# Kernel tuning notes

Measured on AMD Instinct MI355X. Metric: run time of the kernel, lower is better.

The kernel has to match this reference:

```python
import jax, jax.numpy as jnp
import numpy as np

B, T, M, PH, PW = 4, 8, 128, 48, 48
QD, CD, H, DH = 1024, 768, 8, 64
INNER = H * DH

def layer_norm(x, g, b, eps=1e-5):
    m = x.mean(-1, keepdims=True)
    v = ((x - m) ** 2).mean(-1, keepdims=True)
    return (x - m) * jax.lax.rsqrt(v + eps) * g + b

def setup_inputs():
    key = jax.random.key(0)
    ks = jax.random.split(key, 10)
    x = jax.random.normal(ks[0], (B * T, PH * PW, QD), jnp.float32)
    context = jax.random.normal(ks[1], (B, M, CD), jnp.float32)
    sg_node_positions = jax.random.normal(ks[2], (B, M, 3), jnp.float32) * 2.0
    # valid c2w: identity rotation + random translation (invertible)
    c2w = jnp.broadcast_to(jnp.eye(4, dtype=jnp.float32), (B, T, 4, 4))
    camera_c2w = c2w.at[..., :3, 3].set(jax.random.normal(ks[3], (B, T, 3), jnp.float32))
    intrinsics = jnp.broadcast_to(jnp.array([[1.0, 0.0, 0.5], [0.0, 1.0, 0.5], [0.0, 0.0, 1.0]], jnp.float32), (B, 3, 3))
    s = 0.02
    Wq = jax.random.normal(ks[4], (QD, INNER), jnp.float32) * s
    Wk = jax.random.normal(ks[5], (CD, INNER), jnp.float32) * s
    Wv = jax.random.normal(ks[6], (CD, INNER), jnp.float32) * s
    Wo = jax.random.normal(ks[7], (INNER, QD), jnp.float32) * s
    gate = jnp.array([0.1], jnp.float32)          # zero-init in module; nonzero so path is active
    spatial_gate = jnp.array([0.1], jnp.float32)
    spatial_log_sigma = jax.random.normal(ks[8], (H,), jnp.float32) * 0.1
    depth_log_alpha = jax.random.normal(ks[9], (H,), jnp.float32) * 0.1
    gamma_q = jnp.ones((QD,), jnp.float32); beta_q = jnp.zeros((QD,), jnp.float32)
    gamma_k = jnp.ones((CD,), jnp.float32); beta_k = jnp.zeros((CD,), jnp.float32)
    return dict(x=x, context=context, sg_node_positions=sg_node_positions, camera_c2w=camera_c2w,
                intrinsics=intrinsics, Wq=Wq, Wk=Wk, Wv=Wv, Wo=Wo, gate=gate, spatial_gate=spatial_gate,
                spatial_log_sigma=spatial_log_sigma, depth_log_alpha=depth_log_alpha,
                gamma_q=gamma_q, beta_q=beta_q, gamma_k=gamma_k, beta_k=beta_k,
                patch_h=PH, patch_w=PW)

def spatial_bias(sg_node_positions, camera_c2w, intrinsics, spatial_log_sigma, depth_log_alpha, patch_h, patch_w):
    Bb, Mn, _ = sg_node_positions.shape
    Tn = camera_c2w.shape[1]
    w2c = jnp.linalg.inv(camera_c2w)
    R = w2c[:, :, :3, :3]
    tv = w2c[:, :, :3, 3]
    p_cam = jnp.einsum('btij,bmj->btmi', R, sg_node_positions) + tv[:, :, None, :]  # (B,T,M,3)
    z = jnp.clip(p_cam[..., 2], 1e-4, None)
    fx = intrinsics[:, 0, 0]; fy = intrinsics[:, 1, 1]
    cx = intrinsics[:, 0, 2]; cy = intrinsics[:, 1, 2]
    u = fx[:, None, None] * (p_cam[..., 0] / z) + cx[:, None, None]   # (B,T,M)
    v = fy[:, None, None] * (p_cam[..., 1] / z) + cy[:, None, None]
    gy = (jnp.arange(patch_h, dtype=jnp.float32) + 0.5) / patch_h
    gx = (jnp.arange(patch_w, dtype=jnp.float32) + 0.5) / patch_w
    gyy, gxx = jnp.meshgrid(gy, gx, indexing='ij')
    gxx = gxx.reshape(-1); gyy = gyy.reshape(-1)                       # (P,)
    sq = (gxx[None, None, :, None] - u[:, :, None, :]) ** 2 + (gyy[None, None, :, None] - v[:, :, None, :]) ** 2  # (B,T,P,M)
    sigma = jnp.exp(spatial_log_sigma)
    inv2s = z[:, :, None, :] ** 2 / (2.0 * sigma[None, None, :, None] ** 2 + 1e-8)  # (B,T,H,M)
    bias = -sq[:, :, None, :, :] * inv2s[:, :, :, None, :]             # (B,T,H,P,M)
    depth_term = depth_log_alpha[None, None, :, None, None] * (-jnp.log(z))[:, :, None, None, :]
    bias = bias + depth_term
    behind = p_cam[..., 2] <= 0.0
    bias = jnp.where(behind[:, :, None, None, :], 0.0, bias)
    return bias.reshape(Bb * Tn, bias.shape[2], patch_h * patch_w, Mn)  # (BT,H,P,M)

def reference(x, context, sg_node_positions, camera_c2w, intrinsics, Wq, Wk, Wv, Wo, gate, spatial_gate,
              spatial_log_sigma, depth_log_alpha, gamma_q, beta_q, gamma_k, beta_k, patch_h, patch_w):
    BT, P, _ = x.shape
    Bb, Mn, _ = context.shape
    Tn = camera_c2w.shape[1]
    q = layer_norm(x, gamma_q, beta_q) @ Wq                            # (BT,P,INNER)
    ck = layer_norm(context, gamma_k, beta_k)
    k = ck @ Wk
    v = ck @ Wv
    q = q.reshape(BT, P, H, DH).transpose(0, 2, 1, 3)                  # (BT,H,P,DH)
    k = jnp.broadcast_to(k.reshape(Bb, 1, Mn, H, DH), (Bb, Tn, Mn, H, DH)).reshape(BT, Mn, H, DH).transpose(0, 2, 1, 3)
    v = jnp.broadcast_to(v.reshape(Bb, 1, Mn, H, DH), (Bb, Tn, Mn, H, DH)).reshape(BT, Mn, H, DH).transpose(0, 2, 1, 3)
    scores = jnp.einsum('bhpd,bhmd->bhpm', q, k) * (DH ** -0.5)        # (BT,H,P,M)
    bias = spatial_bias(sg_node_positions, camera_c2w, intrinsics, spatial_log_sigma, depth_log_alpha, patch_h, patch_w)
    scores = scores + jnp.tanh(spatial_gate) * bias
    attn = jax.nn.softmax(scores, axis=-1)
    out = jnp.einsum('bhpm,bhmd->bhpd', attn, v).transpose(0, 2, 1, 3).reshape(BT, P, INNER)
    return x + jnp.tanh(gate) * (out @ Wo)
```

## Files before the change

### kernel.cpp

```cpp
#include <hip/hip_runtime.h>
#include <hip/hip_bf16.h>
#include <stdint.h>
#include <cstddef>

typedef short short8 __attribute__((ext_vector_type(8)));
typedef float f32x4 __attribute__((ext_vector_type(4)));
typedef unsigned short us4 __attribute__((ext_vector_type(4)));
typedef unsigned short us8 __attribute__((ext_vector_type(8)));

#define DEV static __device__ __forceinline__

DEV unsigned short f2b(float f) {
  __hip_bfloat16 h = __float2bfloat16(f);
  return __builtin_bit_cast(unsigned short, h);
}

DEV void gload_lds16(const void* g, void* lds) {
  __builtin_amdgcn_global_load_lds((const __attribute__((address_space(1))) unsigned int*)g,
                                   (__attribute__((address_space(3))) unsigned int*)lds, 16, 0, 0);
}

template<int EPI>
__launch_bounds__(256, 2)
__global__ void gemm_bt(const unsigned short* __restrict__ A,
                        const unsigned short* __restrict__ Bt,
                        unsigned short* __restrict__ Cb,
                        float* __restrict__ Cf,
                        const float* __restrict__ xres,
                        const float* __restrict__ gatep,
                        int M, int N, int K)
{
  __shared__ __attribute__((aligned(16))) char As[16384];
  __shared__ __attribute__((aligned(16))) char Bs[16384];
  const int tid  = threadIdx.x;
  const int lane = tid & 63, w = tid >> 6;
  const int wr = w >> 1, wc = w & 1;
  const int g = lane >> 4, lr = lane & 15;
  const int ntile = N >> 7;
  const int nwg = gridDim.x;
  const int bid = blockIdx.x;
  const int tile = ((nwg & 7) == 0) ? ((bid & 7)*(nwg >> 3) + (bid >> 3)) : bid;
  const int m0 = (tile / ntile) << 7;
  const int n0 = (tile % ntile) << 7;

  const int lrow  = lane >> 3;
  const int lslot = (lane & 7) ^ lrow;

  f32x4 acc[4][4] = {};

  for (int k0 = 0; k0 < K; k0 += 64) {
#pragma unroll
    for (int c = 0; c < 4; ++c) {
      const int rowc = (w*4 + c)*8;
      gload_lds16(A  + (size_t)(m0 + rowc + lrow)*K + k0 + lslot*8, As + rowc*128);
      gload_lds16(Bt + (size_t)(n0 + rowc + lrow)*K + k0 + lslot*8, Bs + rowc*128);
    }
    __syncthreads();
#pragma unroll
    for (int ks = 0; ks < 2; ++ks) {
      short8 af[4], bfr[4];
#pragma unroll
      for (int mt = 0; mt < 4; ++mt) {
        int row = wr*64 + mt*16 + lr;
        int slot = (ks*4 + g) ^ (row & 7);
        af[mt] = *(const short8*)(As + row*128 + slot*16);
      }
#pragma unroll
      for (int nt = 0; nt < 4; ++nt) {
        int row = wc*64 + nt*16 + lr;
        int slot = (ks*4 + g) ^ (row & 7);
        bfr[nt] = *(const short8*)(Bs + row*128 + slot*16);
      }
#pragma unroll
      for (int mt = 0; mt < 4; ++mt)
#pragma unroll
        for (int nt = 0; nt < 4; ++nt)
          acc[mt][nt] = __builtin_amdgcn_mfma_f32_16x16x32_bf16(af[mt], bfr[nt], acc[mt][nt], 0, 0, 0);
    }
    __syncthreads();
  }

  float* Sw = (float*)(As) + w*1024;
  if (EPI == 1) {
    const float tg = tanhf(gatep[0]);
#pragma unroll
    for (int mt = 0; mt < 4; ++mt) {
#pragma unroll
      for (int nt = 0; nt < 4; ++nt)
#pragma unroll
        for (int r = 0; r < 4; ++r)
          Sw[(g*4 + r)*64 + nt*16 + lr] = acc[mt][nt][r];
#pragma unroll
      for (int rep = 0; rep < 4; ++rep) {
        int row2 = rep*4 + g;
        int colf = lr*4;
        f32x4 val = *(const f32x4*)(Sw + row2*64 + colf);
        size_t rowg = (size_t)(m0 + wr*64 + mt*16 + row2);
        size_t idx = rowg * (size_t)N + (n0 + wc*64 + colf);
        f32x4 xv = *(const f32x4*)(xres + idx);
#pragma unroll
        for (int j = 0; j < 4; ++j) val[j] = xv[j] + tg*val[j];
        *(f32x4*)(Cf + idx) = val;
      }
    }
  } else {
#pragma unroll
    for (int mt = 0; mt < 4; ++mt) {
#pragma unroll
      for (int nt = 0; nt < 4; ++nt)
#pragma unroll
        for (int r = 0; r < 4; ++r)
          Sw[(g*4 + r)*64 + nt*16 + lr] = acc[mt][nt][r];
#pragma unroll
      for (int rep = 0; rep < 2; ++rep) {
        int row2 = rep*8 + (lane >> 3);
        int colf = (lane & 7)*8;
        f32x4 a0 = *(const f32x4*)(Sw + row2*64 + colf);
        f32x4 a1 = *(const f32x4*)(Sw + row2*64 + colf + 4);
        us8 ov;
#pragma unroll
        for (int j = 0; j < 4; ++j) { ov[j] = f2b(a0[j]); ov[4+j] = f2b(a1[j]); }
        size_t rowg = (size_t)(m0 + wr*64 + mt*16 + row2);
        *(us8*)(Cb + rowg * (size_t)N + (n0 + wc*64 + colf)) = ov;
      }
    }
  }
}

__launch_bounds__(256, 2)
__global__ void gemm_kv(const unsigned short* __restrict__ ck,
                        const unsigned short* __restrict__ Wk_t,
                        const unsigned short* __restrict__ Wv_t,
                        unsigned short* __restrict__ Kb,
                        unsigned short* __restrict__ Vt)
{
  __shared__ __attribute__((aligned(16))) char As[16384];
  __shared__ __attribute__((aligned(16))) char Bs[16384];
  const int bid = blockIdx.x;
  const int kv = bid >> 4, bidl = bid & 15;
  const unsigned short* Bt = kv ? Wv_t : Wk_t;
  const int m0 = (bidl >> 2) << 7, n0 = (bidl & 3) << 7;
  const int tid  = threadIdx.x;
  const int lane = tid & 63, w = tid >> 6;
  const int wr = w >> 1, wc = w & 1;
  const int g = lane >> 4, lr = lane & 15;
  const int lrow  = lane >> 3;
  const int lslot = (lane & 7) ^ lrow;
  const int K = 768;

  f32x4 acc[4][4] = {};

  for (int k0 = 0; k0 < K; k0 += 64) {
#pragma unroll
    for (int c = 0; c < 4; ++c) {
      const int rowc = (w*4 + c)*8;
      gload_lds16(ck + (size_t)(m0 + rowc + lrow)*K + k0 + lslot*8, As + rowc*128);
      gload_lds16(Bt + (size_t)(n0 + rowc + lrow)*K + k0 + lslot*8, Bs + rowc*128);
    }
    __syncthreads();
#pragma unroll
    for (int ks = 0; ks < 2; ++ks) {
      short8 af[4], bfr[4];
#pragma unroll
      for (int mt = 0; mt < 4; ++mt) {
        int row = wr*64 + mt*16 + lr;
        int slot = (ks*4 + g) ^ (row & 7);
        af[mt] = *(const short8*)(As + row*128 + slot*16);
      }
#pragma unroll
      for (int nt = 0; nt < 4; ++nt) {
        int row = wc*64 + nt*16 + lr;
        int slot = (ks*4 + g) ^ (row & 7);
        bfr[nt] = *(const short8*)(Bs + row*128 + slot*16);
      }
#pragma unroll
      for (int mt = 0; mt < 4; ++mt)
#pragma unroll
        for (int nt = 0; nt < 4; ++nt)
          acc[mt][nt] = __builtin_amdgcn_mfma_f32_16x16x32_bf16(af[mt], bfr[nt], acc[mt][nt], 0, 0, 0);
    }
    __syncthreads();
  }

#pragma unroll
  for (int mt = 0; mt < 4; ++mt)
#pragma unroll
    for (int nt = 0; nt < 4; ++nt)
#pragma unroll
      for (int r = 0; r < 4; ++r) {
        int row = m0 + wr*64 + mt*16 + g*4 + r;
        int col = n0 + wc*64 + nt*16 + lr;
        int bb = row >> 7, mm = row & 127, hh = col >> 6, dd = col & 63;
        unsigned short val = f2b(acc[mt][nt][r]);
        if (kv == 0) Kb[(((size_t)(bb*8 + hh))*128 + mm)*64 + dd] = val;
        else         Vt[(((size_t)(bb*8 + hh))*64 + dd)*128 + mm] = val;
      }
}

template<int NSEG>
__global__ void ln_rows(const float* __restrict__ in, const float* __restrict__ gamma,
                        const float* __restrict__ beta, unsigned short* __restrict__ out, int C)
{
  const int lane = threadIdx.x & 63;
  const size_t row = (size_t)blockIdx.x*4 + (threadIdx.x >> 6);
  const float* rp = in + row * (size_t)C;
  f32x4 vals[NSEG];
  float s = 0.f, sq = 0.f;
#pragma unroll
  for (int i = 0; i < NSEG; ++i) {
    f32x4 v = *(const f32x4*)(rp + (i*64 + lane)*4);
    vals[i] = v;
#pragma unroll
    for (int j = 0; j < 4; ++j) { s += v[j]; sq += v[j]*v[j]; }
  }
#pragma unroll
  for (int off = 32; off >= 1; off >>= 1) {
    s  += __shfl_xor(s, off);
    sq += __shfl_xor(sq, off);
  }
  const float invC = 1.0f / (float)C;
  float mean = s * invC;
  float var  = sq * invC - mean*mean;
  float rstd = rsqrtf(var + 1e-5f);
#pragma unroll
  for (int i = 0; i < NSEG; ++i) {
    int cb = (i*64 + lane)*4;
    f32x4 gm = *(const f32x4*)(gamma + cb);
    f32x4 bb = *(const f32x4*)(beta + cb);
    us4 ov;
#pragma unroll
    for (int j = 0; j < 4; ++j)
      ov[j] = f2b((vals[i][j] - mean)*rstd*gm[j] + bb[j]);
    *(us4*)(out + row * (size_t)C + cb) = ov;
  }
}

__global__ void transpose_all(const float* __restrict__ Wq, const float* __restrict__ Wk,
                              const float* __restrict__ Wv, const float* __restrict__ Wo,
                              unsigned short* __restrict__ Wq_t, unsigned short* __restrict__ Wk_t,
                              unsigned short* __restrict__ Wv_t, unsigned short* __restrict__ Wo_t)
{
  __shared__ float tile[32][33];
  int bidx = blockIdx.x;
  const float* src; unsigned short* dst; int R, C;
  if (bidx < 512)       { src = Wq; dst = Wq_t; R = 1024; C = 512; }
  else if (bidx < 896)  { src = Wk; dst = Wk_t; R = 768;  C = 512;  bidx -= 512; }
  else if (bidx < 1280) { src = Wv; dst = Wv_t; R = 768;  C = 512;  bidx -= 896; }
  else                  { src = Wo; dst = Wo_t; R = 512;  C = 1024; bidx -= 1280; }
  const int cb = C >> 5;
  const int bx = bidx % cb, by = bidx / cb;
  const int tx = threadIdx.x & 31, ty = threadIdx.x >> 5;
#pragma unroll
  for (int i = 0; i < 32; i += 8)
    tile[ty + i][tx] = src[(size_t)(by*32 + ty + i)*C + bx*32 + tx];
  __syncthreads();
#pragma unroll
  for (int i = 0; i < 32; i += 8)
    dst[(size_t)(bx*32 + ty + i)*R + by*32 + tx] = f2b(tile[tx][ty + i]);
}

__global__ void spatial_pre(const float* __restrict__ pos, const float* __restrict__ c2w,
                            const float* __restrict__ intr, const float* __restrict__ sls,
                            const float* __restrict__ dla,
                            float* __restrict__ u_o, float* __restrict__ v_o, float* __restrict__ bh_o,
                            float* __restrict__ iv_o, float* __restrict__ dp_o)
{
  const int bt = blockIdx.x;
  const int b = bt >> 3;
  const int m = threadIdx.x;
  const float* Mc = c2w + (size_t)bt*16;
  float r00=Mc[0], r01=Mc[1], r02=Mc[2],  t0=Mc[3];
  float r10=Mc[4], r11=Mc[5], r12=Mc[6],  t1=Mc[7];
  float r20=Mc[8], r21=Mc[9], r22=Mc[10], t2=Mc[11];
  float a00 = r11*r22 - r12*r21;
  float a01 = r02*r21 - r01*r22;
  float a02 = r01*r12 - r02*r11;
  float a10 = r12*r20 - r10*r22;
  float a11 = r00*r22 - r02*r20;
  float a12 = r02*r10 - r00*r12;
  float a20 = r10*r21 - r11*r20;
  float a21 = r01*r20 - r00*r21;
  float a22 = r00*r11 - r01*r10;
  float det = r00*a00 + r01*a10 + r02*a20;
  float id = 1.0f/det;
  a00*=id; a01*=id; a02*=id; a10*=id; a11*=id; a12*=id; a20*=id; a21*=id; a22*=id;
  float tv0 = -(a00*t0 + a01*t1 + a02*t2);
  float tv1 = -(a10*t0 + a11*t1 + a12*t2);
  float tv2 = -(a20*t0 + a21*t1 + a22*t2);
  const float* pm = pos + (size_t)(b*128 + m)*3;
  float px = pm[0], py = pm[1], pz = pm[2];
  float x = a00*px + a01*py + a02*pz + tv0;
  float y = a10*px + a11*py + a12*pz + tv1;
  float zraw = a20*px + a21*py + a22*pz + tv2;
  float z = fmaxf(zraw, 1e-4f);
  float fx = intr[b*9 + 0], fy = intr[b*9 + 4], cx = intr[b*9 + 2], cy = intr[b*9 + 5];
  u_o[bt*128 + m] = fx*(x/z) + cx;
  v_o[bt*128 + m] = fy*(y/z) + cy;
  bh_o[bt*128 + m] = (zraw <= 0.0f) ? 1.0f : 0.0f;
  float lz = __logf(z);
#pragma unroll
  for (int hh = 0; hh < 8; ++hh) {
    float sg = __expf(sls[hh]);
    iv_o[(size_t)(bt*8 + hh)*128 + m] = z*z / (2.0f*sg*sg + 1e-8f);
    dp_o[(size_t)(bt*8 + hh)*128 + m] = dla[hh] * (-lz);
  }
}

__launch_bounds__(256, 2)
__global__ void attn_kernel(const unsigned short* __restrict__ q,
                            const unsigned short* __restrict__ Kb,
                            const unsigned short* __restrict__ Vt,
                            const float* __restrict__ ub, const float* __restrict__ vb,
                            const float* __restrict__ bhb,
                            const float* __restrict__ ivb, const float* __restrict__ dpb,
                            const float* __restrict__ sgate,
                            unsigned short* __restrict__ out)
{
  const int bid = blockIdx.x;
  const int ptile = bid % 18;
  const int h  = (bid / 18) & 7;
  const int bt = bid / (18*8);
  const int b  = bt >> 3;
  const int lane = threadIdx.x & 63, w = threadIdx.x >> 6;
  const int g = lane >> 4, lr = lane & 15;
  const int p0 = ptile*128 + w*32;

  const float sg = tanhf(sgate[0]);
  const unsigned short* Kh = Kb + ((size_t)(b*8 + h)) * (128*64);
  const unsigned short* Vh = Vt + ((size_t)(b*8 + h)) * (64*128);
  const unsigned short* qh = q + (size_t)bt*2304*512 + h*64;

  short8 qf[2][2];
#pragma unroll
  for (int pt = 0; pt < 2; ++pt)
#pragma unroll
    for (int ks = 0; ks < 2; ++ks)
      qf[pt][ks] = *(const short8*)(qh + (size_t)(p0 + pt*16 + lr)*512 + ks*32 + g*8);

  f32x4 st[8][2] = {};
#pragma unroll
  for (int mt = 0; mt < 8; ++mt) {
#pragma unroll
    for (int ks = 0; ks < 2; ++ks) {
      short8 kf = *(const short8*)(Kh + (mt*16 + lr)*64 + ks*32 + g*8);
#pragma unroll
      for (int pt = 0; pt < 2; ++pt)
        st[mt][pt] = __builtin_amdgcn_mfma_f32_16x16x32_bf16(kf, qf[pt][ks], st[mt][pt], 0, 0, 0);
    }
  }

  float gx[2], gy[2];
#pragma unroll
  for (int pt = 0; pt < 2; ++pt) {
    int p = p0 + pt*16 + lr;
    int py = p / 48, px = p - py*48;
    gx[pt] = (px + 0.5f) * (1.0f/48.0f);
    gy[pt] = (py + 0.5f) * (1.0f/48.0f);
  }
  const float* uB = ub  + bt*128;
  const float* vB = vb  + bt*128;
  const float* bB = bhb + bt*128;
  const float* iB = ivb + (size_t)(bt*8 + h)*128;
  const float* dB = dpb + (size_t)(bt*8 + h)*128;

  float pmax[2] = {-3.0e38f, -3.0e38f};
#pragma unroll
  for (int mt = 0; mt < 8; ++mt) {
    int mb = mt*16 + g*4;
    f32x4 uu = *(const f32x4*)(uB + mb);
    f32x4 vv = *(const f32x4*)(vB + mb);
    f32x4 bh = *(const f32x4*)(bB + mb);
    f32x4 iv = *(const f32x4*)(iB + mb);
    f32x4 dp = *(const f32x4*)(dB + mb);
#pragma unroll
    for (int r = 0; r < 4; ++r) {
#pragma unroll
      for (int pt = 0; pt < 2; ++pt) {
        float du = gx[pt] - uu[r], dv = gy[pt] - vv[r];
        float bias = (bh[r] != 0.0f) ? 0.0f : (-(du*du + dv*dv)*iv[r] + dp[r]);
        float s = st[mt][pt][r]*0.125f + sg*bias;
        st[mt][pt][r] = s;
        pmax[pt] = fmaxf(pmax[pt], s);
      }
    }
  }
#pragma unroll
  for (int pt = 0; pt < 2; ++pt) {
    pmax[pt] = fmaxf(pmax[pt], __shfl_xor(pmax[pt], 16));
    pmax[pt] = fmaxf(pmax[pt], __shfl_xor(pmax[pt], 32));
  }
  float psum[2] = {0.f, 0.f};
#pragma unroll
  for (int mt = 0; mt < 8; ++mt)
#pragma unroll
    for (int pt = 0; pt < 2; ++pt)
#pragma unroll
      for (int r = 0; r < 4; ++r) {
        float e = __expf(st[mt][pt][r] - pmax[pt]);
        st[mt][pt][r] = e;
        psum[pt] += e;
      }
#pragma unroll
  for (int pt = 0; pt < 2; ++pt) {
    psum[pt] += __shfl_xor(psum[pt], 16);
    psum[pt] += __shfl_xor(psum[pt], 32);
  }
  float pinv[2] = {1.0f/psum[0], 1.0f/psum[1]};

  short8 pf[2][4];
#pragma unroll
  for (int pt = 0; pt < 2; ++pt)
#pragma unroll
    for (int ms = 0; ms < 4; ++ms)
#pragma unroll
      for (int i = 0; i < 8; ++i)
        pf[pt][ms][i] = (short)f2b(st[ms*2 + (i>>2)][pt][i & 3] * pinv[pt]);

  f32x4 o[4][2] = {};
#pragma unroll
  for (int ms = 0; ms < 4; ++ms) {
#pragma unroll
    for (int dt = 0; dt < 4; ++dt) {
      const unsigned short* vp = Vh + (size_t)(dt*16 + lr)*128 + ms*32 + g*4;
      us4 v0 = *(const us4*)(vp);
      us4 v1 = *(const us4*)(vp + 16);
      short8 vf;
#pragma unroll
      for (int i = 0; i < 4; ++i) { vf[i] = (short)v0[i]; vf[i+4] = (short)v1[i]; }
#pragma unroll
      for (int pt = 0; pt < 2; ++pt)
        o[dt][pt] = __builtin_amdgcn_mfma_f32_16x16x32_bf16(vf, pf[pt][ms], o[dt][pt], 0, 0, 0);
    }
  }

#pragma unroll
  for (int dt = 0; dt < 4; ++dt)
#pragma unroll
    for (int pt = 0; pt < 2; ++pt) {
      int p = p0 + pt*16 + lr;
      int d = h*64 + dt*16 + g*4;
      us4 ov;
#pragma unroll
      for (int r = 0; r < 4; ++r) ov[r] = f2b(o[dt][pt][r]);
      *(us4*)(out + (size_t)(bt*2304 + p)*512 + d) = ov;
    }
}

extern "C" void kernel_launch(void* const* d_in, const int* in_sizes, int n_in,
                              void* d_out, int out_size, void* d_ws, size_t ws_size,
                              hipStream_t stream)
{
  const float* x     = (const float*)d_in[0];
  const float* ctx   = (const float*)d_in[1];
  const float* pos   = (const float*)d_in[2];
  const float* c2w   = (const float*)d_in[3];
  const float* intr  = (const float*)d_in[4];
  const float* Wq    = (const float*)d_in[5];
  const float* Wk    = (const float*)d_in[6];
  const float* Wv    = (const float*)d_in[7];
  const float* Wo    = (const float*)d_in[8];
  const float* gate  = (const float*)d_in[9];
  const float* sgate = (const float*)d_in[10];
  const float* sls   = (const float*)d_in[11];
  const float* dla   = (const float*)d_in[12];
  const float* gq    = (const float*)d_in[13];
  const float* bq    = (const float*)d_in[14];
  const float* gk    = (const float*)d_in[15];
  const float* bk    = (const float*)d_in[16];

  char* ws = (char*)d_ws;
  size_t off = 0;
  auto alloc = [&](size_t bytes) {
    char* p = ws + off;
    off += (bytes + 255) & ~(size_t)255;
    return p;
  };
  unsigned short* ln_x  = (unsigned short*)alloc(73728ull*1024*2);
  unsigned short* qbuf  = (unsigned short*)alloc(73728ull*512*2);
  unsigned short* Wq_t  = (unsigned short*)alloc(512ull*1024*2);
  unsigned short* Wk_t  = (unsigned short*)alloc(512ull*768*2);
  unsigned short* Wv_t  = (unsigned short*)alloc(512ull*768*2);
  unsigned short* Wo_t  = (unsigned short*)alloc(1024ull*512*2);
  unsigned short* ck    = (unsigned short*)alloc(512ull*768*2);
  unsigned short* Kbuf  = (unsigned short*)alloc(4ull*8*128*64*2);
  unsigned short* Vtb   = (unsigned short*)alloc(4ull*8*64*128*2);
  float* u_o  = (float*)alloc(32*128*4);
  float* v_o  = (float*)alloc(32*128*4);
  float* bh_o = (float*)alloc(32*128*4);
  float* iv_o = (float*)alloc(32ull*8*128*4);
  float* dp_o = (float*)alloc(32ull*8*128*4);
  unsigned short* attn_out = ln_x;

  transpose_all<<<1792, 256, 0, stream>>>(Wq, Wk, Wv, Wo, Wq_t, Wk_t, Wv_t, Wo_t);

  ln_rows<4><<<73728/4, 256, 0, stream>>>(x, gq, bq, ln_x, 1024);
  ln_rows<3><<<512/4,   256, 0, stream>>>(ctx, gk, bk, ck, 768);

  spatial_pre<<<32, 128, 0, stream>>>(pos, c2w, intr, sls, dla, u_o, v_o, bh_o, iv_o, dp_o);

  gemm_kv<<<32, 256, 0, stream>>>(ck, Wk_t, Wv_t, Kbuf, Vtb);

  gemm_bt<0><<<(73728/128)*(512/128), 256, 0, stream>>>(ln_x, Wq_t, qbuf, nullptr, nullptr, nullptr, 73728, 512, 1024);

  attn_kernel<<<32*8*18, 256, 0, stream>>>(qbuf, Kbuf, Vtb, u_o, v_o, bh_o, iv_o, dp_o, sgate, attn_out);

  gemm_bt<1><<<(73728/128)*(1024/128), 256, 0, stream>>>(attn_out, Wo_t, nullptr, (float*)d_out, x, gate, 73728, 1024, 512);
}
```

Before: 506.7 us.

## Use 256x256 double-buffered GEMM for Q projection and fuse prep kernels

Adds a new 512-thread GEMM kernel with 256x256 output tiles, a two-stage LDS double buffer loaded via direct global-to-LDS loads, XOR-swizzled slots, and an LDS-staged bf16 epilogue with vectorized stores. It replaces the 128x128 kernel for the Q projection to raise operand reuse per block. Separately, it merges weight transposes, context layer norm and spatial precompute into one launch to cut launch overhead. The large LDS footprint limits occupancy to one block per CU, and the smaller grid may quantize poorly across CUs.

```diff
diff --git a/kernel.cpp b/kernel.cpp
--- a/kernel.cpp
+++ b/kernel.cpp
@@ -18,6 +18,102 @@
 DEV void gload_lds16(const void* g, void* lds) {
   __builtin_amdgcn_global_load_lds((const __attribute__((address_space(1))) unsigned int*)g,
                                    (__attribute__((address_space(3))) unsigned int*)lds, 16, 0, 0);
+}
+
+__launch_bounds__(512, 2)
+__global__ void gemm256(const unsigned short* __restrict__ A,
+                        const unsigned short* __restrict__ Bt,
+                        unsigned short* __restrict__ Cb,
+                        int M, int N, int K)
+{
+  __shared__ __attribute__((aligned(16))) char lds[131072];
+  const int tid  = threadIdx.x;
+  const int lane = tid & 63, w = tid >> 6;
+  const int wr = w >> 2, wc = w & 3;
+  const int g = lane >> 4, lr = lane & 15;
+  const int lrow  = lane >> 3;
+  const int lslot = (lane & 7) ^ lrow;
+
+  const int ntile = N >> 8;
+  const int nwg = gridDim.x;
+  const int bid = blockIdx.x;
+  const int tile = ((nwg & 7) == 0) ? ((bid & 7)*(nwg >> 3) + (bid >> 3)) : bid;
+  const size_t m0 = (size_t)(tile / ntile) << 8;
+  const size_t n0 = (size_t)(tile % ntile) << 8;
+
+  f32x4 acc[8][4] = {};
+
+  auto STAGE = [&](int k0, int bufsel) {
+    char* Ad = lds + bufsel*65536 + w*1024;
+    char* Bd = Ad + 32768;
+#pragma unroll
+    for (int j = 0; j < 4; ++j) {
+      const int row = j*64 + w*8 + lrow;
+      gload_lds16(A  + (m0 + row)*(size_t)K + k0 + lslot*8, Ad + j*8192);
+      gload_lds16(Bt + (n0 + row)*(size_t)K + k0 + lslot*8, Bd + j*8192);
+    }
+  };
+
+  STAGE(0, 0);
+  STAGE(64, 1);
+
+  const int NT = K >> 6;
+  for (int t = 0; t < NT; ++t) {
+    const int cur = t & 1;
+    if (t + 1 < NT) { asm volatile("s_waitcnt vmcnt(8)" ::: "memory"); }
+    else            { asm volatile("s_waitcnt vmcnt(0)" ::: "memory"); }
+    __builtin_amdgcn_s_barrier();
+    __builtin_amdgcn_sched_barrier(0);
+
+    const char* Ab = lds + cur*65536;
+    const char* Bb = Ab + 32768;
+#pragma unroll
+    for (int ks = 0; ks < 2; ++ks) {
+      short8 bfr[4];
+#pragma unroll
+      for (int nt = 0; nt < 4; ++nt) {
+        const int row = wc*64 + nt*16 + lr;
+        const int slot = (ks*4 + g) ^ (row & 7);
+        bfr[nt] = *(const short8*)(Bb + row*128 + slot*16);
+      }
+#pragma unroll
+      for (int mt = 0; mt < 8; ++mt) {
+        const int row = wr*128 + mt*16 + lr;
+        const int slot = (ks*4 + g) ^ (row & 7);
+        short8 af = *(const short8*)(Ab + row*128 + slot*16);
+#pragma unroll
+        for (int nt = 0; nt < 4; ++nt)
+          acc[mt][nt] = __builtin_amdgcn_mfma_f32_16x16x32_bf16(af, bfr[nt], acc[mt][nt], 0, 0, 0);
+      }
+    }
+
+    __builtin_amdgcn_sched_barrier(0);
+    __builtin_amdgcn_s_barrier();
+    __builtin_amdgcn_sched_barrier(0);
+    if (t + 2 < NT) STAGE((t + 2) << 6, cur);
+  }
+
+  float* Sw = (float*)(lds) + w*1024;
+#pragma unroll
+  for (int mt = 0; mt < 8; ++mt) {
+#pragma unroll
+    for (int nt = 0; nt < 4; ++nt)
+#pragma unroll
+      for (int r = 0; r < 4; ++r)
+        Sw[(g*4 + r)*64 + nt*16 + lr] = acc[mt][nt][r];
+#pragma unroll
+    for (int rep = 0; rep < 2; ++rep) {
+      const int row2 = rep*8 + (lane >> 3);
+      const int colf = (lane & 7)*8;
+      f32x4 a0 = *(const f32x4*)(Sw + row2*64 + colf);
+      f32x4 a1 = *(const f32x4*)(Sw + row2*64 + colf + 4);
+      us8 ov;
+#pragma unroll
+      for (int j = 0; j < 4; ++j) { ov[j] = f2b(a0[j]); ov[4+j] = f2b(a1[j]); }
+      const size_t rowg = m0 + wr*128 + mt*16 + row2;
+      *(us8*)(Cb + rowg * (size_t)N + (n0 + wc*64 + colf)) = ov;
+    }
+  }
 }
 
 template<int EPI>
@@ -198,11 +294,12 @@
 }
 
 template<int NSEG>
-__global__ void ln_rows(const float* __restrict__ in, const float* __restrict__ gamma,
-                        const float* __restrict__ beta, unsigned short* __restrict__ out, int C)
-{
-  const int lane = threadIdx.x & 63;
-  const size_t row = (size_t)blockIdx.x*4 + (threadIdx.x >> 6);
+DEV void ln_rows_body(const float* __restrict__ in, const float* __restrict__ gamma,
+                      const float* __restrict__ beta, unsigned short* __restrict__ out,
+                      int C, int blk, int tid)
+{
+  const int lane = tid & 63;
+  const size_t row = (size_t)blk*4 + (tid >> 6);
   const float* rp = in + row * (size_t)C;
   f32x4 vals[NSEG];
   float s = 0.f, sq = 0.f;
@@ -235,37 +332,50 @@
   }
 }
 
-__global__ void transpose_all(const float* __restrict__ Wq, const float* __restrict__ Wk,
-                              const float* __restrict__ Wv, const float* __restrict__ Wo,
-                              unsigned short* __restrict__ Wq_t, unsigned short* __restrict__ Wk_t,
-                              unsigned short* __restrict__ Wv_t, unsigned short* __restrict__ Wo_t)
+__global__ void ln_big(const float* __restrict__ in, const float* __restrict__ gamma,
+                       const float* __restrict__ beta, unsigned short* __restrict__ out)
+{
+  ln_rows_body<4>(in, gamma, beta, out, 1024, blockIdx.x, threadIdx.x);
+}
+
+__global__ void prep(const float* __restrict__ Wq, const float* __restrict__ Wk,
+                     const float* __restrict__ Wv, const float* __restrict__ Wo,
+                     unsigned short* __restrict__ Wq_t, unsigned short* __restrict__ Wk_t,
+                     unsigned short* __restrict__ Wv_t, unsigned short* __restrict__ Wo_t,
+                     const float* __restrict__ ctx, const float* __restrict__ gk,
+                     const float* __restrict__ bk, unsigned short* __restrict__ ck,
+                     const float* __restrict__ pos, const float* __restrict__ c2w,
+                     const float* __restrict__ intr, const float* __restrict__ sls,
+                     const float* __restrict__ dla,
+                     float* __restrict__ u_o, float* __restrict__ v_o, float* __restrict__ bh_o,
+                     float* __restrict__ iv_o, float* __restrict__ dp_o)
 {
   __shared__ float tile[32][33];
   int bidx = blockIdx.x;
-  const float* src; unsigned short* dst; int R, C;
-  if (bidx < 512)       { src = Wq; dst = Wq_t; R = 1024; C = 512; }
-  else if (bidx < 896)  { src = Wk; dst = Wk_t; R = 768;  C = 512;  bidx -= 512; }
-  else if (bidx < 1280) { src = Wv; dst = Wv_t; R = 768;  C = 512;  bidx -= 896; }
-  else                  { src = Wo; dst = Wo_t; R = 512;  C = 1024; bidx -= 1280; }
-  const int cb = C >> 5;
-  const int bx = bidx % cb, by = bidx / cb;
-  const int tx = threadIdx.x & 31, ty = threadIdx.x >> 5;
-#pragma unroll
-  for (int i = 0; i < 32; i += 8)
-    tile[ty + i][tx] = src[(size_t)(by*32 + ty + i)*C + bx*32 + tx];
-  __syncthreads();
-#pragma unroll
-  for (int i = 0; i < 32; i += 8)
-    dst[(size_t)(bx*32 + ty + i)*R + by*32 + tx] = f2b(tile[tx][ty + i]);
-}
-
-__global__ void spatial_pre(const float* __restrict__ pos, const float* __restrict__ c2w,
-                            const float* __restrict__ intr, const float* __restrict__ sls,
-                            const float* __restrict__ dla,
-                            float* __restrict__ u_o, float* __restrict__ v_o, float* __restrict__ bh_o,
-                            float* __restrict__ iv_o, float* __restrict__ dp_o)
-{
-  const int bt = blockIdx.x;
+  if (bidx < 1792) {
+    const float* src; unsigned short* dst; int R, C;
+    if (bidx < 512)       { src = Wq; dst = Wq_t; R = 1024; C = 512; }
+    else if (bidx < 896)  { src = Wk; dst = Wk_t; R = 768;  C = 512;  bidx -= 512; }
+    else if (bidx < 1280) { src = Wv; dst = Wv_t; R = 768;  C = 512;  bidx -= 896; }
+    else                  { src = Wo; dst = Wo_t; R = 512;  C = 1024; bidx -= 1280; }
+    const int cb = C >> 5;
+    const int bx = bidx % cb, by = bidx / cb;
+    const int tx = threadIdx.x & 31, ty = threadIdx.x >> 5;
+#pragma unroll
+    for (int i = 0; i < 32; i += 8)
+      tile[ty + i][tx] = src[(size_t)(by*32 + ty + i)*C + bx*32 + tx];
+    __syncthreads();
+#pragma unroll
+    for (int i = 0; i < 32; i += 8)
+      dst[(size_t)(bx*32 + ty + i)*R + by*32 + tx] = f2b(tile[tx][ty + i]);
+    return;
+  }
+  if (bidx < 1920) {
+    ln_rows_body<3>(ctx, gk, bk, ck, 768, bidx - 1792, threadIdx.x);
+    return;
+  }
+  if (threadIdx.x >= 128) return;
+  const int bt = bidx - 1920;
   const int b = bt >> 3;
   const int m = threadIdx.x;
   const float* Mc = c2w + (size_t)bt*16;
@@ -491,16 +601,16 @@
   float* dp_o = (float*)alloc(32ull*8*128*4);
   unsigned short* attn_out = ln_x;
 
-  transpose_all<<<1792, 256, 0, stream>>>(Wq, Wk, Wv, Wo, Wq_t, Wk_t, Wv_t, Wo_t);
-
-  ln_rows<4><<<73728/4, 256, 0, stream>>>(x, gq, bq, ln_x, 1024);
-  ln_rows<3><<<512/4,   256, 0, stream>>>(ctx, gk, bk, ck, 768);
-
-  spatial_pre<<<32, 128, 0, stream>>>(pos, c2w, intr, sls, dla, u_o, v_o, bh_o, iv_o, dp_o);
+  prep<<<1952, 256, 0, stream>>>(Wq, Wk, Wv, Wo, Wq_t, Wk_t, Wv_t, Wo_t,
+                                 ctx, gk, bk, ck,
+                                 pos, c2w, intr, sls, dla,
+                                 u_o, v_o, bh_o, iv_o, dp_o);
+
+  ln_big<<<73728/4, 256, 0, stream>>>(x, gq, bq, ln_x);
 
   gemm_kv<<<32, 256, 0, stream>>>(ck, Wk_t, Wv_t, Kbuf, Vtb);
 
-  gemm_bt<0><<<(73728/128)*(512/128), 256, 0, stream>>>(ln_x, Wq_t, qbuf, nullptr, nullptr, nullptr, 73728, 512, 1024);
+  gemm256<<<(73728/256)*(512/256), 512, 0, stream>>>(ln_x, Wq_t, qbuf, 73728, 512, 1024);
 
   attn_kernel<<<32*8*18, 256, 0, stream>>>(qbuf, Kbuf, Vtb, u_o, v_o, bh_o, iv_o, dp_o, sgate, attn_out);
 
```

After: 510.9 us. About the same (+0.8%).
